# Performance work log

Measured on AMD Instinct MI355X. Metric: run time of the kernel, lower is better.

The kernel has to match this reference:

```python
import jax, jax.numpy as jnp
import numpy as np

P_FWD = 0.95


def setup_inputs() -> dict:
    key = jax.random.key(0)
    k1, k2, k3 = jax.random.split(key, 3)
    B, IN, OUT = 8192, 4096, 4096
    inputs = jax.random.normal(k1, (B, IN), dtype=jnp.float32)
    weight = jax.random.normal(k2, (OUT, IN), dtype=jnp.float32)
    bias = jax.random.normal(k3, (OUT,), dtype=jnp.float32)
    return {"inputs": inputs, "weight": weight, "bias": bias}


def reference(inputs, weight, bias):
    # TopKAST forward mask: keep weights with |w| >= quantile(|w|, p_forward)
    absw = jnp.abs(weight)
    thr = jnp.quantile(absw.reshape(-1), P_FWD)
    w_fwd = jnp.where(absw >= thr, weight, jnp.zeros((), weight.dtype))
    # sparse.addmm(bias[:,None], W_sparse, x.T).T == x @ W_masked.T + bias
    return inputs @ w_fwd.T + bias
```

## Files before the change

kernel.cpp:

```cpp
#include <hip/hip_runtime.h>
#include <stdint.h>

typedef unsigned short ushort_t;

#define M_DIM 8192
#define N_DIM 4096
#define K_DIM 4096
#define N_W   (N_DIM * K_DIM)
#define RANK_LO 15938354
#define RANK_HI 15938355

#define WS_CTRL   0u
#define WS_H1     1024u
#define WS_H2A    16384u
#define WS_H2B    (16384u + 262144u)
#define WS_LISTA  540672u
#define WS_LISTB  544768u
#define WS_ZERO_BYTES 540672u
#define WS_ABF    (1u << 20)
#define WS_WBF    ((1u << 20) + 67108864u)
#define WS_NEED   ((size_t)(1u << 20) + 67108864u + 33554432u)

#define C_C0 0
#define C_R0 1
#define C_C1 2
#define C_R1 3
#define C_M0 4
#define C_R0B 5
#define C_M1 6
#define C_R1B 7
#define C_CNTA 8
#define C_CNTB 9
#define C_TBITS 10

__device__ __forceinline__ ushort_t f2bf(float f) {
    uint32_t x = __float_as_uint(f);
    uint32_t r = (x + 0x7FFFu + ((x >> 16) & 1u)) >> 16;
    return (ushort_t)r;
}


__global__ void k_hist1(const uint32_t* __restrict__ w, uint32_t* __restrict__ h1) {
    __shared__ uint32_t lh[2048];
    for (int i = threadIdx.x; i < 2048; i += 256) lh[i] = 0;
    __syncthreads();
    const uint4* w4 = (const uint4*)w;
    const int n4 = N_W / 4;
    for (int i = blockIdx.x * 256 + threadIdx.x; i < n4; i += gridDim.x * 256) {
        uint4 v = w4[i];
        atomicAdd(&lh[(v.x & 0x7FFFFFFFu) >> 20], 1u);
        atomicAdd(&lh[(v.y & 0x7FFFFFFFu) >> 20], 1u);
        atomicAdd(&lh[(v.z & 0x7FFFFFFFu) >> 20], 1u);
        atomicAdd(&lh[(v.w & 0x7FFFFFFFu) >> 20], 1u);
    }
    __syncthreads();
    for (int i = threadIdx.x; i < 2048; i += 256)
        if (lh[i]) atomicAdd(&h1[i], lh[i]);
}

__global__ void k_sel1(const uint32_t* __restrict__ h1, uint32_t* __restrict__ ctrl) {
    __shared__ uint32_t part[256];
    __shared__ uint32_t ex[256];
    int t = threadIdx.x;
    uint32_t loc[8];
    uint32_t s = 0;
    for (int j = 0; j < 8; j++) { loc[j] = h1[t * 8 + j]; s += loc[j]; }
    part[t] = s;
    __syncthreads();
    if (t == 0) { uint32_t c = 0; for (int i = 0; i < 256; i++) { ex[i] = c; c += part[i]; } }
    __syncthreads();
    uint32_t cum = ex[t];
    for (int j = 0; j < 8; j++) {
        uint32_t c = loc[j];
        if (RANK_LO >= cum && RANK_LO < cum + c) { ctrl[C_C0] = t * 8 + j; ctrl[C_R0] = RANK_LO - cum; }
        if (RANK_HI >= cum && RANK_HI < cum + c) { ctrl[C_C1] = t * 8 + j; ctrl[C_R1] = RANK_HI - cum; }
        cum += c;
    }
}

__global__ void k_hist2(const uint32_t* __restrict__ w, const uint32_t* __restrict__ ctrl,
                        uint32_t* __restrict__ h2a, uint32_t* __restrict__ h2b) {
    uint32_t c0 = ctrl[C_C0], c1 = ctrl[C_C1];
    const uint4* w4 = (const uint4*)w;
    const int n4 = N_W / 4;
    for (int i = blockIdx.x * 256 + threadIdx.x; i < n4; i += gridDim.x * 256) {
        uint4 v = w4[i];
        uint32_t u;
        u = v.x & 0x7FFFFFFFu; if ((u >> 20) == c0) atomicAdd(&h2a[(u >> 4) & 0xFFFFu], 1u); if ((u >> 20) == c1) atomicAdd(&h2b[(u >> 4) & 0xFFFFu], 1u);
        u = v.y & 0x7FFFFFFFu; if ((u >> 20) == c0) atomicAdd(&h2a[(u >> 4) & 0xFFFFu], 1u); if ((u >> 20) == c1) atomicAdd(&h2b[(u >> 4) & 0xFFFFu], 1u);
        u = v.z & 0x7FFFFFFFu; if ((u >> 20) == c0) atomicAdd(&h2a[(u >> 4) & 0xFFFFu], 1u); if ((u >> 20) == c1) atomicAdd(&h2b[(u >> 4) & 0xFFFFu], 1u);
        u = v.w & 0x7FFFFFFFu; if ((u >> 20) == c0) atomicAdd(&h2a[(u >> 4) & 0xFFFFu], 1u); if ((u >> 20) == c1) atomicAdd(&h2b[(u >> 4) & 0xFFFFu], 1u);
    }
}

__global__ void k_sel2(const uint32_t* __restrict__ h2a, const uint32_t* __restrict__ h2b,
                       uint32_t* __restrict__ ctrl) {
    __shared__ uint32_t part[256];
    __shared__ uint32_t ex[256];
    int t = threadIdx.x;
    for (int which = 0; which < 2; which++) {
        const uint32_t* h = which ? h2b : h2a;
        uint32_t target = ctrl[which ? C_R1 : C_R0];
        uint32_t s = 0;
        for (int j = 0; j < 256; j++) s += h[t * 256 + j];
        part[t] = s;
        __syncthreads();
        if (t == 0) { uint32_t c = 0; for (int i = 0; i < 256; i++) { ex[i] = c; c += part[i]; } }
        __syncthreads();
        uint32_t cum = ex[t];
        for (int j = 0; j < 256; j++) {
            uint32_t c = h[t * 256 + j];
            if (target >= cum && target < cum + c) {
                ctrl[which ? C_M1 : C_M0]  = t * 256 + j;
                ctrl[which ? C_R1B : C_R0B] = target - cum;
            }
            cum += c;
        }
        __syncthreads();
    }
}

__global__ void k_gather(const uint32_t* __restrict__ w, uint32_t* __restrict__ ctrl,
                         uint32_t* __restrict__ listA, uint32_t* __restrict__ listB) {
    uint32_t keyA = (ctrl[C_C0] << 16) | ctrl[C_M0];
    uint32_t keyB = (ctrl[C_C1] << 16) | ctrl[C_M1];
    const uint4* w4 = (const uint4*)w;
    const int n4 = N_W / 4;
    for (int i = blockIdx.x * 256 + threadIdx.x; i < n4; i += gridDim.x * 256) {
        uint4 v = w4[i];
        uint32_t u;
        u = v.x & 0x7FFFFFFFu;
        if ((u >> 4) == keyA) { uint32_t p = atomicAdd(&ctrl[C_CNTA], 1u); if (p < 1024) listA[p] = u; }
        if ((u >> 4) == keyB) { uint32_t p = atomicAdd(&ctrl[C_CNTB], 1u); if (p < 1024) listB[p] = u; }
        u = v.y & 0x7FFFFFFFu;
        if ((u >> 4) == keyA) { uint32_t p = atomicAdd(&ctrl[C_CNTA], 1u); if (p < 1024) listA[p] = u; }
        if ((u >> 4) == keyB) { uint32_t p = atomicAdd(&ctrl[C_CNTB], 1u); if (p < 1024) listB[p] = u; }
        u = v.z & 0x7FFFFFFFu;
        if ((u >> 4) == keyA) { uint32_t p = atomicAdd(&ctrl[C_CNTA], 1u); if (p < 1024) listA[p] = u; }
        if ((u >> 4) == keyB) { uint32_t p = atomicAdd(&ctrl[C_CNTB], 1u); if (p < 1024) listB[p] = u; }
        u = v.w & 0x7FFFFFFFu;
        if ((u >> 4) == keyA) { uint32_t p = atomicAdd(&ctrl[C_CNTA], 1u); if (p < 1024) listA[p] = u; }
        if ((u >> 4) == keyB) { uint32_t p = atomicAdd(&ctrl[C_CNTB], 1u); if (p < 1024) listB[p] = u; }
    }
}

__global__ void k_final(const uint32_t* __restrict__ listA, const uint32_t* __restrict__ listB,
                        uint32_t* __restrict__ ctrl) {
    __shared__ uint32_t res[2];
    int lane = threadIdx.x;
    for (int which = 0; which < 2; which++) {
        const uint32_t* lst = which ? listB : listA;
        uint32_t n = ctrl[which ? C_CNTB : C_CNTA];
        if (n > 1024u) n = 1024u;
        uint32_t k = ctrl[which ? C_R1B : C_R0B];
        for (uint32_t i = lane; i < n; i += 64) {
            uint32_t x = lst[i];
            uint32_t lo = 0, eq = 0;
            for (uint32_t j = 0; j < n; j++) { uint32_t y = lst[j]; lo += (y < x); eq += (y == x); }
            if (lo <= k && k < lo + eq) res[which] = x;
        }
        __syncthreads();
    }
    if (lane == 0) {
        ctrl[C_TBITS] = res[0];
    }
}


__global__ void k_convA(const float4* __restrict__ x, ushort4* __restrict__ y, int n4) {
    for (int i = blockIdx.x * 256 + threadIdx.x; i < n4; i += gridDim.x * 256) {
        float4 v = x[i];
        ushort4 o;
        o.x = f2bf(v.x); o.y = f2bf(v.y); o.z = f2bf(v.z); o.w = f2bf(v.w);
        y[i] = o;
    }
}

__global__ void k_maskW(const float4* __restrict__ w, const uint32_t* __restrict__ ctrl,
                        ushort4* __restrict__ y, int n4) {
    float T = __uint_as_float(ctrl[C_TBITS]);
    for (int i = blockIdx.x * 256 + threadIdx.x; i < n4; i += gridDim.x * 256) {
        float4 v = w[i];
        ushort4 o;
        o.x = (fabsf(v.x) >= T) ? f2bf(v.x) : (ushort_t)0;
        o.y = (fabsf(v.y) >= T) ? f2bf(v.y) : (ushort_t)0;
        o.z = (fabsf(v.z) >= T) ? f2bf(v.z) : (ushort_t)0;
        o.w = (fabsf(v.w) >= T) ? f2bf(v.w) : (ushort_t)0;
        y[i] = o;
    }
}


typedef __bf16 bf16x8 __attribute__((ext_vector_type(8)));
typedef float  f32x4  __attribute__((ext_vector_type(4)));
typedef short  s16x8  __attribute__((ext_vector_type(8)));

union FragCvt { s16x8 s; bf16x8 b; };

__device__ __forceinline__ void gload_lds16(const void* g, void* lds) {
    __builtin_amdgcn_global_load_lds(
        (const __attribute__((address_space(1))) void*)(uintptr_t)g,
        (__attribute__((address_space(3))) void*)(uintptr_t)lds,
        16, 0, 0);
}

__global__ __launch_bounds__(256) void k_gemm(
    const ushort_t* __restrict__ A, const ushort_t* __restrict__ B,
    const float* __restrict__ bias, float* __restrict__ C) {
    __shared__ __align__(16) short lsA[128 * 32];
    __shared__ __align__(16) short lsB[128 * 32];

    const int tid  = threadIdx.x;
    const int lane = tid & 63;
    const int wid  = tid >> 6;
    const int wm   = wid >> 1, wn = wid & 1;

    int bid = blockIdx.x;
    bid = (bid & 7) * 256 + (bid >> 3);
    const int bm = bid / (N_DIM / 128);
    const int bn = bid % (N_DIM / 128);

    f32x4 acc[4][4] = {};

    const char* gA = (const char*)A + (size_t)bm * 128 * (K_DIM * 2);
    const char* gB = (const char*)B + (size_t)bn * 128 * (K_DIM * 2);
    const int r0 = lane >> 2;
    const int cb = (lane & 3) * 16;
    const int lr = lane & 15;
    const int lk = lane >> 4;

    for (int k0 = 0; k0 < K_DIM; k0 += 32) {
        __syncthreads();
#pragma unroll
        for (int j = 0; j < 2; j++) {
            const int idx = wid * 2 + j;
            const int row = idx * 16 + r0;
            gload_lds16(gA + (size_t)row * (K_DIM * 2) + k0 * 2 + cb, &lsA[idx * 512]);
            gload_lds16(gB + (size_t)row * (K_DIM * 2) + k0 * 2 + cb, &lsB[idx * 512]);
        }
        __syncthreads();

        FragCvt a[4], b[4];
#pragma unroll
        for (int m = 0; m < 4; m++) {
            a[m].s = *(const s16x8*)&lsA[(wm * 64 + m * 16 + lr) * 32 + lk * 8];
            b[m].s = *(const s16x8*)&lsB[(wn * 64 + m * 16 + lr) * 32 + lk * 8];
        }
#pragma unroll
        for (int m = 0; m < 4; m++)
#pragma unroll
            for (int n = 0; n < 4; n++)
                acc[m][n] = __builtin_amdgcn_mfma_f32_16x16x32_bf16(a[m].b, b[n].b, acc[m][n], 0, 0, 0);
    }

    const int colbase = bn * 128 + wn * 64 + lr;
    const int rowbase = bm * 128 + wm * 64 + lk * 4;
#pragma unroll
    for (int n = 0; n < 4; n++) {
        float bv = bias[colbase + n * 16];
#pragma unroll
        for (int m = 0; m < 4; m++) {
#pragma unroll
            for (int r = 0; r < 4; r++)
                C[(size_t)(rowbase + m * 16 + r) * N_DIM + colbase + n * 16] = acc[m][n][r] + bv;
        }
    }
}

__global__ void k_gemm_f32(const float* __restrict__ A, const float* __restrict__ W,
                           const uint32_t* __restrict__ ctrl, const float* __restrict__ bias,
                           float* __restrict__ C) {
    __shared__ float sA[16][64];
    __shared__ float sW[16][65];
    float T = __uint_as_float(ctrl[C_TBITS]);
    int bx = blockIdx.x % (N_DIM / 16), by = blockIdx.x / (N_DIM / 16);
    int tx = threadIdx.x & 15, ty = threadIdx.x >> 4;
    float acc = 0.f;
    for (int k0 = 0; k0 < K_DIM; k0 += 64) {
        for (int j = threadIdx.x; j < 16 * 64; j += 256) {
            int r = j >> 6, c = j & 63;
            sA[r][c] = A[(size_t)(by * 16 + r) * K_DIM + k0 + c];
            float w = W[(size_t)(bx * 16 + r) * K_DIM + k0 + c];
            sW[r][c] = (fabsf(w) >= T) ? w : 0.f;
        }
        __syncthreads();
#pragma unroll 16
        for (int kk = 0; kk < 64; kk++) acc += sA[ty][kk] * sW[tx][kk];
        __syncthreads();
    }
    C[(size_t)(by * 16 + ty) * N_DIM + bx * 16 + tx] = acc + bias[bx * 16 + tx];
}

extern "C" void kernel_launch(void* const* d_in, const int* in_sizes, int n_in,
                              void* d_out, int out_size, void* d_ws, size_t ws_size,
                              hipStream_t stream) {
    const float* x    = (const float*)d_in[0];
    const float* w    = (const float*)d_in[1];
    const float* bias = (const float*)d_in[2];
    float* out = (float*)d_out;
    char* ws = (char*)d_ws;

    uint32_t* ctrl  = (uint32_t*)(ws + WS_CTRL);
    uint32_t* h1    = (uint32_t*)(ws + WS_H1);
    uint32_t* h2a   = (uint32_t*)(ws + WS_H2A);
    uint32_t* h2b   = (uint32_t*)(ws + WS_H2B);
    uint32_t* listA = (uint32_t*)(ws + WS_LISTA);
    uint32_t* listB = (uint32_t*)(ws + WS_LISTB);

    hipMemsetAsync(d_ws, 0, WS_ZERO_BYTES, stream);
    k_hist1 <<<1024, 256, 0, stream>>>((const uint32_t*)w, h1);
    k_sel1  <<<1,    256, 0, stream>>>(h1, ctrl);
    k_hist2 <<<1024, 256, 0, stream>>>((const uint32_t*)w, ctrl, h2a, h2b);
    k_sel2  <<<1,    256, 0, stream>>>(h2a, h2b, ctrl);
    k_gather<<<1024, 256, 0, stream>>>((const uint32_t*)w, ctrl, listA, listB);
    k_final <<<1,     64, 0, stream>>>(listA, listB, ctrl);

    if (ws_size >= WS_NEED) {
        ushort_t* Abf = (ushort_t*)(ws + WS_ABF);
        ushort_t* Wbf = (ushort_t*)(ws + WS_WBF);
        k_convA<<<2048, 256, 0, stream>>>((const float4*)x, (ushort4*)Abf, (M_DIM * K_DIM) / 4);
        k_maskW<<<1024, 256, 0, stream>>>((const float4*)w, ctrl, (ushort4*)Wbf, N_W / 4);
        k_gemm <<<(M_DIM / 128) * (N_DIM / 128), 256, 0, stream>>>(Abf, Wbf, bias, out);
    } else {
        k_gemm_f32<<<(M_DIM / 16) * (N_DIM / 16), 256, 0, stream>>>(x, w, ctrl, bias, out);
    }
}
```

Measured before the change: 753.4 us.

## Rewrite bf16 GEMM with 256x256 tiles, double-buffered LDS and swizzle

Replaces the 128x128 tile GEMM with a 512-thread kernel that computes 256x256 output tiles and uses a 128 KB double-buffered LDS. Each k-slice is split into two 32-wide halves. Global-to-LDS loads for the next slice are issued between MFMA groups, with vmcnt waits and barriers, so loads overlap compute. LDS addresses are XOR-swizzled to avoid bank conflicts, and s_setprio is raised around the MFMA blocks. The intent is higher arithmetic intensity and latency hiding, at the cost of one block per CU, only 512 blocks, and heavy register use for 32 accumulators per lane.

After: 656.5 us. 12.9% less time.

```diff
diff --git a/kernel.cpp b/kernel.cpp
--- a/kernel.cpp
+++ b/kernel.cpp
@@ -204,67 +204,123 @@
         16, 0, 0);
 }
 
-__global__ __launch_bounds__(256) void k_gemm(
+#define SBAR  __builtin_amdgcn_s_barrier()
+#define WVM4  asm volatile("s_waitcnt vmcnt(4)" ::: "memory")
+
+__global__ __launch_bounds__(512, 1) void k_gemm256(
     const ushort_t* __restrict__ A, const ushort_t* __restrict__ B,
     const float* __restrict__ bias, float* __restrict__ C) {
-    __shared__ __align__(16) short lsA[128 * 32];
-    __shared__ __align__(16) short lsB[128 * 32];
+    __shared__ __align__(16) short lsg[65536];
 
     const int tid  = threadIdx.x;
+    const int wid  = tid >> 6;
     const int lane = tid & 63;
-    const int wid  = tid >> 6;
-    const int wm   = wid >> 1, wn = wid & 1;
+    const int wm   = wid >> 2;
+    const int wn   = wid & 3;
+    const int lr   = lane & 15;
+    const int lk   = lane >> 4;
+    const int srow = tid >> 2;
+    const int scol = (tid & 3) * 8;
 
     int bid = blockIdx.x;
-    bid = (bid & 7) * 256 + (bid >> 3);
-    const int bm = bid / (N_DIM / 128);
-    const int bn = bid % (N_DIM / 128);
-
-    f32x4 acc[4][4] = {};
-
-    const char* gA = (const char*)A + (size_t)bm * 128 * (K_DIM * 2);
-    const char* gB = (const char*)B + (size_t)bn * 128 * (K_DIM * 2);
-    const int r0 = lane >> 2;
-    const int cb = (lane & 3) * 16;
-    const int lr = lane & 15;
-    const int lk = lane >> 4;
-
-    for (int k0 = 0; k0 < K_DIM; k0 += 32) {
-        __syncthreads();
-#pragma unroll
-        for (int j = 0; j < 2; j++) {
-            const int idx = wid * 2 + j;
-            const int row = idx * 16 + r0;
-            gload_lds16(gA + (size_t)row * (K_DIM * 2) + k0 * 2 + cb, &lsA[idx * 512]);
-            gload_lds16(gB + (size_t)row * (K_DIM * 2) + k0 * 2 + cb, &lsB[idx * 512]);
-        }
-        __syncthreads();
-
+    bid = (bid & 7) * 64 + (bid >> 3);
+    const int bm = bid >> 4;
+    const int bn = bid & 15;
+
+    const ushort_t* gA = A + (size_t)bm * 256 * K_DIM;
+    const ushort_t* gB = B + (size_t)bn * 256 * K_DIM;
+
+    f32x4 acc[8][4] = {};
+
+    #define STAGE(dbuf, ab, kh, kt, G)                                          \
+        _Pragma("unroll")                                                       \
+        for (int s = 0; s < 2; s++) {                                           \
+            int row = s * 128 + srow;                                           \
+            int col = scol ^ (((row >> 1) & 3) << 3);                           \
+            const ushort_t* src = (G) + (size_t)row * K_DIM + (kt) * 64 + (kh) * 32 + col; \
+            gload_lds16(src, &lsg[(dbuf) * 32768 + (ab) * 16384 + (kh) * 8192 + s * 4096 + wid * 512]); \
+        }
+
+    #define LDA4(dst, dbuf, kh, mbase)                                          \
+        _Pragma("unroll")                                                       \
+        for (int m = 0; m < 4; m++) {                                           \
+            int row = wm * 128 + ((mbase) + m) * 16 + lr;                       \
+            int col = (lk * 8) ^ (((row >> 1) & 3) << 3);                       \
+            dst[m].s = *(const s16x8*)&lsg[(dbuf) * 32768 + (kh) * 8192 + row * 32 + col]; \
+        }
+
+    #define LDB4(dst, dbuf, kh)                                                 \
+        _Pragma("unroll")                                                       \
+        for (int n = 0; n < 4; n++) {                                           \
+            int row = wn * 64 + n * 16 + lr;                                    \
+            int col = (lk * 8) ^ (((row >> 1) & 3) << 3);                       \
+            dst[n].s = *(const s16x8*)&lsg[(dbuf) * 32768 + 16384 + (kh) * 8192 + row * 32 + col]; \
+        }
+
+    #define MM16(af, bf, mbase)                                                 \
+        __builtin_amdgcn_s_setprio(1);                                          \
+        _Pragma("unroll")                                                       \
+        for (int m = 0; m < 4; m++)                                             \
+            _Pragma("unroll")                                                   \
+            for (int n = 0; n < 4; n++)                                         \
+                acc[(mbase) + m][n] = __builtin_amdgcn_mfma_f32_16x16x32_bf16(  \
+                    af[m].b, bf[n].b, acc[(mbase) + m][n], 0, 0, 0);            \
+        __builtin_amdgcn_s_setprio(0);
+
+    STAGE(0, 0, 0, 0, gA); STAGE(0, 1, 0, 0, gB);
+    STAGE(0, 0, 1, 0, gA); STAGE(0, 1, 1, 0, gB);
+    WVM4;
+    SBAR;
+
+    for (int t = 0; t < 64; t++) {
+        const int cur = t & 1, nxt = cur ^ 1;
+        const int ktn = (t + 1) & 63;
         FragCvt a[4], b[4];
-#pragma unroll
-        for (int m = 0; m < 4; m++) {
-            a[m].s = *(const s16x8*)&lsA[(wm * 64 + m * 16 + lr) * 32 + lk * 8];
-            b[m].s = *(const s16x8*)&lsB[(wn * 64 + m * 16 + lr) * 32 + lk * 8];
-        }
-#pragma unroll
-        for (int m = 0; m < 4; m++)
-#pragma unroll
-            for (int n = 0; n < 4; n++)
-                acc[m][n] = __builtin_amdgcn_mfma_f32_16x16x32_bf16(a[m].b, b[n].b, acc[m][n], 0, 0, 0);
-    }
-
-    const int colbase = bn * 128 + wn * 64 + lr;
-    const int rowbase = bm * 128 + wm * 64 + lk * 4;
-#pragma unroll
+
+        LDA4(a, cur, 0, 0); LDB4(b, cur, 0);
+        STAGE(nxt, 0, 0, ktn, gA);
+        SBAR;
+        MM16(a, b, 0);
+        SBAR;
+
+        LDA4(a, cur, 0, 4);
+        STAGE(nxt, 1, 0, ktn, gB);
+        WVM4;
+        SBAR;
+        MM16(a, b, 4);
+        SBAR;
+
+        LDA4(a, cur, 1, 0); LDB4(b, cur, 1);
+        STAGE(nxt, 0, 1, ktn, gA);
+        SBAR;
+        MM16(a, b, 0);
+        SBAR;
+
+        LDA4(a, cur, 1, 4);
+        STAGE(nxt, 1, 1, ktn, gB);
+        WVM4;
+        SBAR;
+        MM16(a, b, 4);
+        SBAR;
+    }
+    asm volatile("s_waitcnt vmcnt(0)" ::: "memory");
+
+    const int colbase = bn * 256 + wn * 64 + lr;
+    const int rowbase = bm * 256 + wm * 128 + lk * 4;
+    #pragma unroll
     for (int n = 0; n < 4; n++) {
         float bv = bias[colbase + n * 16];
-#pragma unroll
-        for (int m = 0; m < 4; m++) {
-#pragma unroll
+        #pragma unroll
+        for (int m = 0; m < 8; m++) {
+            #pragma unroll
             for (int r = 0; r < 4; r++)
                 C[(size_t)(rowbase + m * 16 + r) * N_DIM + colbase + n * 16] = acc[m][n][r] + bv;
         }
     }
+    #undef STAGE
+    #undef LDA4
+    #undef LDB4
+    #undef MM16
 }
 
 __global__ void k_gemm_f32(const float* __restrict__ A, const float* __restrict__ W,
@@ -320,7 +376,7 @@
         ushort_t* Wbf = (ushort_t*)(ws + WS_WBF);
         k_convA<<<2048, 256, 0, stream>>>((const float4*)x, (ushort4*)Abf, (M_DIM * K_DIM) / 4);
         k_maskW<<<1024, 256, 0, stream>>>((const float4*)w, ctrl, (ushort4*)Wbf, N_W / 4);
-        k_gemm <<<(M_DIM / 128) * (N_DIM / 128), 256, 0, stream>>>(Abf, Wbf, bias, out);
+        k_gemm256<<<(M_DIM / 256) * (N_DIM / 256), 512, 0, stream>>>(Abf, Wbf, bias, out);
     } else {
         k_gemm_f32<<<(M_DIM / 16) * (N_DIM / 16), 256, 0, stream>>>(x, w, ctrl, bias, out);
     }
```
